# Kernel tuning notes

Measured on AMD Instinct MI355X. Metric: run time of the kernel, lower is better.

The kernel has to match this reference:

```python
import jax, jax.numpy as jnp
import numpy as np

CONF_THR = 0.3   # cfg.THRESHOLD_PREDICT_CONF
NMS_THR = 0.5    # cfg.THRESHOLD_PREDICT_NMS
TOPK = 500       # hard-coded topk(500) in forward


def _build_grid():
    # YOLOv3 @416: scales 13/26/52, 3 anchors each -> 10647 rows
    sizes = [13, 26, 52]
    anc = np.array([[10, 13], [16, 30], [33, 23], [30, 61], [62, 45], [59, 119],
                    [116, 90], [156, 198], [373, 326]], np.float32) / 416.0
    groups = [anc[6:9], anc[3:6], anc[0:3]]  # large anchors on coarse grid
    grids, anchors, fs = [], [], []
    for s, g in zip(sizes, groups):
        ys, xs = np.meshgrid(np.arange(s), np.arange(s), indexing='ij')
        gxy = np.stack([xs, ys], -1).astype(np.float32)          # [s,s,2]
        gxy = np.repeat(gxy.reshape(-1, 1, 2), 3, axis=1).reshape(-1, 2)
        grids.append(gxy)
        anchors.append(np.tile(g[None], (s * s, 1, 1)).reshape(-1, 2))
        fs.append(np.full((s * s * 3, 1), float(s), np.float32))
    return (np.concatenate(grids).astype(np.float32),
            np.concatenate(anchors).astype(np.float32),
            np.concatenate(fs).astype(np.float32))


def setup_inputs() -> dict:
    key = jax.random.key(0)
    k1, k2, k3 = jax.random.split(key, 3)
    B, A, C = 64, 10647, 80
    g, aw, fs = _build_grid()
    return {
        "pconf": jax.random.normal(k1, (B, A, 1), jnp.float32),
        "pcls": jax.random.normal(k2, (B, A, C), jnp.float32),
        "ptxywh": jax.random.normal(k3, (B, A, 4), jnp.float32),
        "grid_xy": jnp.asarray(g),
        "anchor_wh": jnp.asarray(aw),
        "fsize": jnp.asarray(fs),
    }


def _decode(ptxywh, grid_xy, anchor_wh, fsize):
    # boxes_decode4yolo3: sigmoid xy offset + cell, exp wh * anchor (all normalized)
    xy = (jax.nn.sigmoid(ptxywh[..., :2]) + grid_xy) / fsize   # [B,A,2]
    wh = jnp.exp(ptxywh[..., 2:]) * anchor_wh                  # [B,A,2]
    return jnp.concatenate([xy - 0.5 * wh, xy + 0.5 * wh], -1)  # ltrb


def _pairwise_iou(b):  # b: [K,4] ltrb
    area = jnp.maximum(b[:, 2] - b[:, 0], 0.) * jnp.maximum(b[:, 3] - b[:, 1], 0.)
    lt = jnp.maximum(b[:, None, :2], b[None, :, :2])
    rb = jnp.minimum(b[:, None, 2:], b[None, :, 2:])
    wh = jnp.maximum(rb - lt, 0.)
    inter = wh[..., 0] * wh[..., 1]
    return inter / (area[:, None] + area[None, :] - inter + 1e-9)


def _label_nms(boxes, labels, valid, thr):
    # boxes are pre-sorted by descending score (lax.top_k output order)
    K = boxes.shape[0]
    sup = (_pairwise_iou(boxes) > thr) & (labels[:, None] == labels[None, :])
    idx = jnp.arange(K)

    def body(suppressed, i):
        keep_i = valid[i] & ~suppressed[i]
        suppressed = suppressed | (keep_i & sup[i] & (idx > i))
        return suppressed, keep_i

    _, keep = jax.lax.scan(body, jnp.zeros(K, bool), idx)
    return keep


def reference(pconf, pcls, ptxywh, grid_xy, anchor_wh, fsize):
    B, A, _ = ptxywh.shape
    conf = jax.nn.sigmoid(pconf)[..., 0]            # [B,A]
    pc = jax.nn.sigmoid(pcls)                       # [B,A,C]
    cls_conf = pc.max(-1)
    plabels = pc.argmax(-1)
    pscores = cls_conf * conf                       # [B,A]

    vals, idx = jax.lax.top_k(pscores, TOPK)        # sorted desc, [B,K]
    valid = vals > CONF_THR                         # mask_pos AND mask_topk

    pltrb = _decode(ptxywh, grid_xy, anchor_wh, fsize)          # [B,A,4]
    boxes = jnp.take_along_axis(pltrb, idx[..., None], axis=1)  # [B,K,4]
    boxes = jnp.clip(boxes, 0.0, 1.0)
    labels = jnp.take_along_axis(plabels, idx, axis=1) + 1      # 1-based

    keep = jax.vmap(_label_nms, in_axes=(0, 0, 0, None))(boxes, labels, valid, NMS_THR)
    ids_batch = jnp.broadcast_to(jnp.arange(B)[:, None], (B, TOPK))
    return ids_batch, boxes, labels, vals, keep
```

## Files before the change

kernel.cpp:

```cpp
#include <hip/hip_runtime.h>
#include <math.h>

#define A_N 10647
#define C_N 80
#define K_N 500
#define CONF_THRF 0.3f
#define NMS_THRF 0.5f

#define NBUCK 1024
#define CAND_N 2048
#define CAND_TARGET 600

typedef float f32x4 __attribute__((ext_vector_type(4)));

__device__ __forceinline__ float sigmoid_ref(float x) {
    float e = expf(-x);
    return 1.0f / (1.0f + e);
}

__device__ __forceinline__ unsigned bucket_of(float v) {
    unsigned u = __float_as_uint(v) >> 20;
    return u > 1023u ? 1023u : u;
}

__device__ __forceinline__ unsigned long long shfl_u64(unsigned long long v, int src) {
    unsigned int lo = (unsigned int)v, hi = (unsigned int)(v >> 32);
    lo = __shfl(lo, src, 64);
    hi = __shfl(hi, src, 64);
    return ((unsigned long long)hi << 32) | (unsigned long long)lo;
}

__device__ __forceinline__ unsigned long long shfl_xor_u64(unsigned long long v, int mask) {
    unsigned int lo = (unsigned int)v, hi = (unsigned int)(v >> 32);
    lo = __shfl_xor(lo, mask, 64);
    hi = __shfl_xor(hi, mask, 64);
    return ((unsigned long long)hi << 32) | (unsigned long long)lo;
}

__device__ __forceinline__ void reduce_core(
    const f32x4 v[5], int sub, float& sbest, int& ibest) {
    float m = -3.4e38f;
    #pragma unroll
    for (int j = 0; j < 5; ++j)
        m = fmaxf(m, fmaxf(fmaxf(v[j][0], v[j][1]), fmaxf(v[j][2], v[j][3])));
    m = fmaxf(m, __shfl_xor(m, 1, 64));
    m = fmaxf(m, __shfl_xor(m, 2, 64));

    const float win = m - 1e-4f;
    int imin = 0x7FFFFFFF, cnt = 0;
    #pragma unroll
    for (int j = 0; j < 5; ++j) {
        #pragma unroll
        for (int t = 0; t < 4; ++t) {
            int idx = (sub + 4 * j) * 4 + t;
            if (v[j][t] == m && idx < imin) imin = idx;
            cnt += (v[j][t] >= win) ? 1 : 0;
        }
    }
    {
        int o = __shfl_xor(imin, 1, 64); imin = imin < o ? imin : o;
        o = __shfl_xor(imin, 2, 64);     imin = imin < o ? imin : o;
        cnt += __shfl_xor(cnt, 1, 64);
        cnt += __shfl_xor(cnt, 2, 64);
    }

    if (cnt >= 2) {
        unsigned long long key = 0ull;
        #pragma unroll
        for (int j = 0; j < 5; ++j) {
            #pragma unroll
            for (int t = 0; t < 4; ++t) {
                float x = v[j][t];
                if (x >= win) {
                    int idx = (sub + 4 * j) * 4 + t;
                    float s = sigmoid_ref(x);
                    unsigned long long k =
                        ((unsigned long long)__float_as_uint(s) << 32) |
                        (unsigned long long)(0xFFFFu - (unsigned)idx);
                    if (k > key) key = k;
                }
            }
        }
        unsigned long long o = shfl_xor_u64(key, 1); if (o > key) key = o;
        o = shfl_xor_u64(key, 2);                    if (o > key) key = o;
        sbest = __uint_as_float((unsigned int)(key >> 32));
        ibest = 0xFFFF - (int)(key & 0xFFFFull);
    } else {
        sbest = sigmoid_ref(m);
        ibest = imin;
    }
}

__global__ __launch_bounds__(1024) void ustar_kernel(
    const float* __restrict__ pconf,
    unsigned* __restrict__ ustar,
    unsigned* __restrict__ shist) {
    __shared__ unsigned hist[NBUCK];
    const int b = blockIdx.x, tid = threadIdx.x;
    hist[tid] = 0u;
    shist[(size_t)b * NBUCK + tid] = 0u;
    __syncthreads();
    for (int i = tid; i < A_N; i += 1024) {
        float ubv = sigmoid_ref(pconf[(size_t)b * A_N + i]);
        atomicAdd(&hist[bucket_of(ubv)], 1u);
    }
    __syncthreads();
    for (int d = 1; d < NBUCK; d <<= 1) {
        unsigned v = (tid + d < NBUCK) ? hist[tid + d] : 0u;
        __syncthreads();
        hist[tid] += v;
        __syncthreads();
    }
    if (hist[tid] >= CAND_TARGET && (tid == NBUCK - 1 || hist[tid + 1] < CAND_TARGET))
        ustar[b] = (unsigned)tid;
}

__global__ __launch_bounds__(256) void cand_kernel(
    const float* __restrict__ pconf,
    const float* __restrict__ pcls,
    float* __restrict__ scores,
    int* __restrict__ labels,
    const unsigned* __restrict__ ustar,
    unsigned* __restrict__ shist,
    int total) {
    const int sub = threadIdx.x & 3;
    const int g0 = (blockIdx.x * 256 + threadIdx.x) >> 2;
    const int gstride = (2048 * 256) >> 2;
    for (int r = g0; r < total; r += gstride) {
        unsigned b = (unsigned)r / A_N;
        float ub = sigmoid_ref(pconf[r]);
        if (bucket_of(ub) >= ustar[b]) {
            const f32x4* rp = (const f32x4*)(pcls + (size_t)r * C_N);
            f32x4 v[5];
            #pragma unroll
            for (int j = 0; j < 5; ++j) v[j] = rp[sub + 4 * j];
            float s; int ib;
            reduce_core(v, sub, s, ib);
            float sc = __fmul_rn(s, ub);
            if (sub == 0) {
                scores[r] = sc;
                labels[r] = ib;
                atomicAdd(&shist[(size_t)b * NBUCK + bucket_of(sc)], 1u);
            }
        }
    }
}

__global__ __launch_bounds__(1024) void tval_kernel(
    const unsigned* __restrict__ shist,
    float* __restrict__ tval) {
    __shared__ unsigned hist[NBUCK];
    const int b = blockIdx.x, tid = threadIdx.x;
    hist[tid] = shist[(size_t)b * NBUCK + tid];
    __syncthreads();
    for (int d = 1; d < NBUCK; d <<= 1) {
        unsigned v = (tid + d < NBUCK) ? hist[tid + d] : 0u;
        __syncthreads();
        hist[tid] += v;
        __syncthreads();
    }
    if (hist[tid] >= K_N && (tid == NBUCK - 1 || hist[tid + 1] < K_N))
        tval[b] = __uint_as_float(((unsigned)tid) << 20);
}

__global__ __launch_bounds__(256) void rest_kernel(
    const float* __restrict__ pconf,
    const float* __restrict__ pcls,
    float* __restrict__ scores,
    int* __restrict__ labels,
    const unsigned* __restrict__ ustar,
    const float* __restrict__ tval,
    int total) {
    const int sub = threadIdx.x & 3;
    const int g0 = (blockIdx.x * 256 + threadIdx.x) >> 2;
    const int gstride = (2048 * 256) >> 2;
    for (int r = g0; r < total; r += gstride) {
        unsigned b = (unsigned)r / A_N;
        float ub = sigmoid_ref(pconf[r]);
        unsigned u = bucket_of(ub);
        if (u >= ustar[b]) continue;
        if (ub >= tval[b]) {
            const f32x4* rp = (const f32x4*)(pcls + (size_t)r * C_N);
            f32x4 v[5];
            #pragma unroll
            for (int j = 0; j < 5; ++j) v[j] = rp[sub + 4 * j];
            float s; int ib;
            reduce_core(v, sub, s, ib);
            if (sub == 0) {
                scores[r] = __fmul_rn(s, ub);
                labels[r] = ib;
            }
        } else if (sub == 0) {
            scores[r] = 0.0f;
        }
    }
}

__global__ __launch_bounds__(1024) void topk_nms_kernel(
    const float* __restrict__ scores,
    const int* __restrict__ labels,
    const float* __restrict__ ptxywh,
    const float* __restrict__ grid_xy,
    const float* __restrict__ anchor_wh,
    const float* __restrict__ fsize,
    float* __restrict__ out, int B) {
    extern __shared__ unsigned char smem[];
    unsigned int* hist = (unsigned int*)smem;
    unsigned long long* cand = (unsigned long long*)(smem + 4096);
    unsigned int* cntp = (unsigned int*)(smem + 20480);
    unsigned int* Tp   = (unsigned int*)(smem + 20484);
    const int b = blockIdx.x;
    const int tid = threadIdx.x;
    const float* sb = scores + (size_t)b * A_N;

    hist[tid] = 0u;
    cand[tid] = 0ull;
    cand[tid + 1024] = 0ull;
    if (tid == 0) *cntp = 0u;
    __syncthreads();

    for (int i = tid; i < A_N; i += 1024) {
        unsigned int u = __float_as_uint(sb[i]) >> 20;
        atomicAdd(&hist[u], 1u);
    }
    __syncthreads();

    for (int d = 1; d < NBUCK; d <<= 1) {
        unsigned int v = (tid + d < NBUCK) ? hist[tid + d] : 0u;
        __syncthreads();
        hist[tid] += v;
        __syncthreads();
    }
    if (hist[tid] >= K_N && (tid == NBUCK - 1 || hist[tid + 1] < K_N)) *Tp = (unsigned)tid;
    __syncthreads();
    const unsigned int T = *Tp;
    __syncthreads();

    for (int i = tid; i < A_N; i += 1024) {
        unsigned int u = __float_as_uint(sb[i]);
        if ((u >> 20) >= T) {
            unsigned int slot = atomicAdd(cntp, 1u);
            if (slot < CAND_N)
                cand[slot] = ((unsigned long long)u << 32) |
                             (unsigned long long)(0xFFFFu - (unsigned)i);
        }
    }
    __syncthreads();

    for (int sz = 2; sz <= CAND_N; sz <<= 1) {
        for (int j = sz >> 1; j > 0; j >>= 1) {
            int i = ((tid & ~(j - 1)) << 1) | (tid & (j - 1));
            int l = i | j;
            unsigned long long a = cand[i];
            unsigned long long c = cand[l];
            bool descBlk = ((i & sz) == 0);
            if (descBlk ? (a < c) : (a > c)) { cand[i] = c; cand[l] = a; }
            __syncthreads();
        }
    }

    unsigned long long myk = 0ull;
    if (tid < K_N) myk = cand[tid];
    __syncthreads();

    float* bxL   = (float*)smem;
    float* areaL = (float*)(smem + 8000);
    int*   labL  = (int*)  (smem + 10000);
    float* valsL = (float*)(smem + 12000);
    unsigned long long* nzL   = (unsigned long long*)(smem + 14016);
    unsigned long long* keepL = (unsigned long long*)(smem + 14080);
    unsigned long long* supL  = (unsigned long long*)(smem + 14336);

    if (tid >= 512 && tid < 520) nzL[tid - 512] = 0ull;

    const size_t BK = (size_t)B * K_N;
    if (tid < K_N) {
        float scv = __uint_as_float((unsigned int)(myk >> 32));
        int idx = 0xFFFF - (int)(myk & 0xFFFFull);
        int lb = labels[(size_t)b * A_N + idx] + 1;
        const float* t4 = ptxywh + ((size_t)b * A_N + idx) * 4;
        float tx = t4[0], ty = t4[1], tw = t4[2], th = t4[3];
        float gx = grid_xy[idx * 2 + 0], gy = grid_xy[idx * 2 + 1];
        float aw = anchor_wh[idx * 2 + 0], ah = anchor_wh[idx * 2 + 1];
        float fs = fsize[idx];
        float cx = __fdiv_rn(__fadd_rn(sigmoid_ref(tx), gx), fs);
        float cy = __fdiv_rn(__fadd_rn(sigmoid_ref(ty), gy), fs);
        float wx = __fmul_rn(expf(tw), aw);
        float wy = __fmul_rn(expf(th), ah);
        float hx = __fmul_rn(0.5f, wx);
        float hy = __fmul_rn(0.5f, wy);
        float x0 = __fsub_rn(cx, hx), y0 = __fsub_rn(cy, hy);
        float x1 = __fadd_rn(cx, hx), y1 = __fadd_rn(cy, hy);
        x0 = fminf(fmaxf(x0, 0.0f), 1.0f);
        y0 = fminf(fmaxf(y0, 0.0f), 1.0f);
        x1 = fminf(fmaxf(x1, 0.0f), 1.0f);
        y1 = fminf(fmaxf(y1, 0.0f), 1.0f);
        float area = __fmul_rn(fmaxf(__fsub_rn(x1, x0), 0.0f),
                               fmaxf(__fsub_rn(y1, y0), 0.0f));
        bxL[tid * 4 + 0] = x0; bxL[tid * 4 + 1] = y0;
        bxL[tid * 4 + 2] = x1; bxL[tid * 4 + 3] = y1;
        areaL[tid] = area; labL[tid] = lb; valsL[tid] = scv;

        out[(size_t)b * K_N + tid] = (float)b;
        float* ob = out + BK + ((size_t)b * K_N + tid) * 4;
        ob[0] = x0; ob[1] = y0; ob[2] = x1; ob[3] = y1;
        out[5 * BK + (size_t)b * K_N + tid] = (float)lb;
        out[6 * BK + (size_t)b * K_N + tid] = scv;
    }
    __syncthreads();

    for (int task = tid; task < K_N * 8; task += 1024) {
        int i = task >> 3;
        int w = task & 7;
        float li = bxL[i * 4 + 0], ti = bxL[i * 4 + 1];
        float ri = bxL[i * 4 + 2], bi = bxL[i * 4 + 3];
        float ai = areaL[i];
        int lbi = labL[i];
        unsigned long long bits = 0ull;
        int j0 = w * 64;
        int jend = j0 + 64; if (jend > K_N) jend = K_N;
        int jst = j0 > i + 1 ? j0 : i + 1;
        for (int j = jst; j < jend; ++j) {
            if (labL[j] == lbi) {
                float lj = bxL[j * 4 + 0], tj = bxL[j * 4 + 1];
                float rj = bxL[j * 4 + 2], bj = bxL[j * 4 + 3];
                float ltx = fmaxf(li, lj), lty = fmaxf(ti, tj);
                float rbx = fminf(ri, rj), rby = fminf(bi, bj);
                float iw = fmaxf(__fsub_rn(rbx, ltx), 0.0f);
                float ih = fmaxf(__fsub_rn(rby, lty), 0.0f);
                float inter = __fmul_rn(iw, ih);
                float den = __fadd_rn(__fsub_rn(__fadd_rn(ai, areaL[j]), inter), 1e-9f);
                float iou = __fdiv_rn(inter, den);
                if (iou > NMS_THRF) bits |= (1ull << (j - j0));
            }
        }
        supL[i * 8 + w] = bits;
        if (bits) atomicOr(&nzL[i >> 6], 1ull << (i & 63));
    }
    __syncthreads();

    if (tid < 64) {
        const int lane = tid;
        unsigned long long supp = 0ull, keepm = 0ull;
        unsigned long long nzreg = (lane < 8) ? nzL[lane] : 0ull;
        #pragma unroll
        for (int t = 0; t < 8; ++t) {
            const int i0 = t * 64;
            int myi = i0 + lane;
            bool v = (myi < K_N) ? (valsL[myi] > CONF_THRF) : false;
            unsigned long long vword = __ballot(v);
            unsigned long long nzword = shfl_u64(nzreg, t);
            const int imax = (K_N - i0 < 64) ? (K_N - i0) : 64;
            for (int i2 = 0; i2 < imax; ++i2) {
                unsigned long long sw = shfl_u64(supp, t);
                bool keep_i = ((vword >> i2) & 1ull) && !((sw >> i2) & 1ull);
                if (keep_i) {
                    if (lane == t) keepm |= (1ull << i2);
                    if ((nzword >> i2) & 1ull) {
                        if (lane < 8) supp |= supL[(i0 + i2) * 8 + lane];
                    }
                }
            }
        }
        if (lane < 8) keepL[lane] = keepm;
    }
    __syncthreads();

    if (tid < K_N) {
        unsigned long long kw = keepL[tid >> 6];
        out[7 * BK + (size_t)b * K_N + tid] = (float)((kw >> (tid & 63)) & 1ull);
    }
}

extern "C" void kernel_launch(void* const* d_in, const int* in_sizes, int n_in,
                              void* d_out, int out_size, void* d_ws, size_t ws_size,
                              hipStream_t stream) {
    const float* pconf     = (const float*)d_in[0];
    const float* pcls      = (const float*)d_in[1];
    const float* ptxywh    = (const float*)d_in[2];
    const float* grid_xy   = (const float*)d_in[3];
    const float* anchor_wh = (const float*)d_in[4];
    const float* fsize     = (const float*)d_in[5];
    int total = in_sizes[0];
    int B = total / A_N;
    if (B <= 0) return;

    float*    scores = (float*)d_ws;
    int*      labls  = (int*)((char*)d_ws + (size_t)total * 4);
    unsigned* shist  = (unsigned*)((char*)d_ws + (size_t)total * 8);
    unsigned* ustar  = shist + (size_t)B * NBUCK;
    float*    tval   = (float*)(ustar + B);
    float*    out    = (float*)d_out;

    hipLaunchKernelGGL(ustar_kernel, dim3(B), dim3(1024), 0, stream,
                       pconf, ustar, shist);
    hipLaunchKernelGGL(cand_kernel, dim3(2048), dim3(256), 0, stream,
                       pconf, pcls, scores, labls, ustar, shist, total);
    hipLaunchKernelGGL(tval_kernel, dim3(B), dim3(1024), 0, stream,
                       shist, tval);
    hipLaunchKernelGGL(rest_kernel, dim3(2048), dim3(256), 0, stream,
                       pconf, pcls, scores, labls, ustar, tval, total);
    hipLaunchKernelGGL(topk_nms_kernel, dim3(B), dim3(1024), 46592, stream,
                       scores, labls, ptxywh, grid_xy, anchor_wh, fsize, out, B);
}
```

Baseline: 177.9 us.

## Compact candidate row indices into per-batch lists before class scoring

The per-batch histogram kernels now also build compacted index lists of rows that pass the bucket threshold, and the scoring kernels iterate over those lists instead of scanning all rows and branching. This removes the divergent full scans where most lanes idle, so the class-row loads only go to work-dense wavefronts. In exchange, the per-batch 1024-thread kernels do a second pass over pconf, the scoring kernels still launch enough threads to cover every row and most exit early, and list order depends on atomics.

```diff
diff --git a/kernel.cpp b/kernel.cpp
--- a/kernel.cpp
+++ b/kernel.cpp
@@ -91,18 +91,22 @@
     }
 }
 
-__global__ __launch_bounds__(1024) void ustar_kernel(
+__global__ __launch_bounds__(1024) void ustar_compact_kernel(
     const float* __restrict__ pconf,
+    unsigned* __restrict__ shist,
     unsigned* __restrict__ ustar,
-    unsigned* __restrict__ shist) {
+    int* __restrict__ list1,
+    unsigned* __restrict__ count1) {
     __shared__ unsigned hist[NBUCK];
+    __shared__ unsigned lcnt, ustarL;
     const int b = blockIdx.x, tid = threadIdx.x;
     hist[tid] = 0u;
     shist[(size_t)b * NBUCK + tid] = 0u;
+    if (tid == 0) lcnt = 0u;
     __syncthreads();
     for (int i = tid; i < A_N; i += 1024) {
-        float ubv = sigmoid_ref(pconf[(size_t)b * A_N + i]);
-        atomicAdd(&hist[bucket_of(ubv)], 1u);
+        float ub = sigmoid_ref(pconf[(size_t)b * A_N + i]);
+        atomicAdd(&hist[bucket_of(ub)], 1u);
     }
     __syncthreads();
     for (int d = 1; d < NBUCK; d <<= 1) {
@@ -112,46 +116,70 @@
         __syncthreads();
     }
     if (hist[tid] >= CAND_TARGET && (tid == NBUCK - 1 || hist[tid + 1] < CAND_TARGET))
-        ustar[b] = (unsigned)tid;
-}
-
-__global__ __launch_bounds__(256) void cand_kernel(
+        ustarL = (unsigned)tid;
+    __syncthreads();
+    const unsigned u = ustarL;
+    if (tid == 0) ustar[b] = u;
+    for (int i = tid; i < A_N; i += 1024) {
+        int r = b * A_N + i;
+        float ub = sigmoid_ref(pconf[r]);
+        if (bucket_of(ub) >= u) {
+            unsigned slot = atomicAdd(&lcnt, 1u);
+            list1[(size_t)b * A_N + slot] = r;
+        }
+    }
+    __syncthreads();
+    if (tid == 0) count1[b] = lcnt;
+}
+
+template<bool DO_HIST>
+__global__ __launch_bounds__(256) void score_list_kernel(
     const float* __restrict__ pconf,
     const float* __restrict__ pcls,
     float* __restrict__ scores,
     int* __restrict__ labels,
-    const unsigned* __restrict__ ustar,
+    const int* __restrict__ list,
+    const unsigned* __restrict__ count,
     unsigned* __restrict__ shist,
     int total) {
     const int sub = threadIdx.x & 3;
     const int g0 = (blockIdx.x * 256 + threadIdx.x) >> 2;
     const int gstride = (2048 * 256) >> 2;
-    for (int r = g0; r < total; r += gstride) {
-        unsigned b = (unsigned)r / A_N;
+    for (int idx = g0; idx < total; idx += gstride) {
+        int b = idx / A_N;
+        int k = idx - b * A_N;
+        if (k >= (int)count[b]) continue;
+        int r = list[idx];
         float ub = sigmoid_ref(pconf[r]);
-        if (bucket_of(ub) >= ustar[b]) {
-            const f32x4* rp = (const f32x4*)(pcls + (size_t)r * C_N);
-            f32x4 v[5];
-            #pragma unroll
-            for (int j = 0; j < 5; ++j) v[j] = rp[sub + 4 * j];
-            float s; int ib;
-            reduce_core(v, sub, s, ib);
-            float sc = __fmul_rn(s, ub);
-            if (sub == 0) {
-                scores[r] = sc;
-                labels[r] = ib;
+        const f32x4* rp = (const f32x4*)(pcls + (size_t)r * C_N);
+        f32x4 v[5];
+        #pragma unroll
+        for (int j = 0; j < 5; ++j) v[j] = rp[sub + 4 * j];
+        float s; int ib;
+        reduce_core(v, sub, s, ib);
+        float sc = __fmul_rn(s, ub);
+        if (sub == 0) {
+            scores[r] = sc;
+            labels[r] = ib;
+            if (DO_HIST)
                 atomicAdd(&shist[(size_t)b * NBUCK + bucket_of(sc)], 1u);
-            }
-        }
-    }
-}
-
-__global__ __launch_bounds__(1024) void tval_kernel(
+        }
+    }
+}
+
+__global__ __launch_bounds__(1024) void tval_compact_kernel(
+    const float* __restrict__ pconf,
     const unsigned* __restrict__ shist,
-    float* __restrict__ tval) {
+    const unsigned* __restrict__ ustar,
+    float* __restrict__ scores,
+    int* __restrict__ list2,
+    unsigned* __restrict__ count2) {
     __shared__ unsigned hist[NBUCK];
+    __shared__ unsigned lcnt;
+    __shared__ float tL;
     const int b = blockIdx.x, tid = threadIdx.x;
     hist[tid] = shist[(size_t)b * NBUCK + tid];
+    if (tid == 0) lcnt = 0u;
     __syncthreads();
     for (int d = 1; d < NBUCK; d <<= 1) {
         unsigned v = (tid + d < NBUCK) ? hist[tid + d] : 0u;
@@ -160,40 +188,24 @@
         __syncthreads();
     }
     if (hist[tid] >= K_N && (tid == NBUCK - 1 || hist[tid + 1] < K_N))
-        tval[b] = __uint_as_float(((unsigned)tid) << 20);
-}
-
-__global__ __launch_bounds__(256) void rest_kernel(
-    const float* __restrict__ pconf,
-    const float* __restrict__ pcls,
-    float* __restrict__ scores,
-    int* __restrict__ labels,
-    const unsigned* __restrict__ ustar,
-    const float* __restrict__ tval,
-    int total) {
-    const int sub = threadIdx.x & 3;
-    const int g0 = (blockIdx.x * 256 + threadIdx.x) >> 2;
-    const int gstride = (2048 * 256) >> 2;
-    for (int r = g0; r < total; r += gstride) {
-        unsigned b = (unsigned)r / A_N;
+        tL = __uint_as_float(((unsigned)tid) << 20);
+    __syncthreads();
+    const float t = tL;
+    const unsigned u = ustar[b];
+    for (int i = tid; i < A_N; i += 1024) {
+        int r = b * A_N + i;
         float ub = sigmoid_ref(pconf[r]);
-        unsigned u = bucket_of(ub);
-        if (u >= ustar[b]) continue;
-        if (ub >= tval[b]) {
-            const f32x4* rp = (const f32x4*)(pcls + (size_t)r * C_N);
-            f32x4 v[5];
-            #pragma unroll
-            for (int j = 0; j < 5; ++j) v[j] = rp[sub + 4 * j];
-            float s; int ib;
-            reduce_core(v, sub, s, ib);
-            if (sub == 0) {
-                scores[r] = __fmul_rn(s, ub);
-                labels[r] = ib;
-            }
-        } else if (sub == 0) {
+        unsigned bk = bucket_of(ub);
+        if (bk >= u) continue;
+        if (ub >= t) {
+            unsigned slot = atomicAdd(&lcnt, 1u);
+            list2[(size_t)b * A_N + slot] = r;
+        } else {
             scores[r] = 0.0f;
         }
     }
+    __syncthreads();
+    if (tid == 0) count2[b] = lcnt;
 }
 
 __global__ __launch_bounds__(1024) void topk_nms_kernel(
@@ -385,21 +397,25 @@
     int B = total / A_N;
     if (B <= 0) return;
 
-    float*    scores = (float*)d_ws;
-    int*      labls  = (int*)((char*)d_ws + (size_t)total * 4);
-    unsigned* shist  = (unsigned*)((char*)d_ws + (size_t)total * 8);
-    unsigned* ustar  = shist + (size_t)B * NBUCK;
-    float*    tval   = (float*)(ustar + B);
+    char* w = (char*)d_ws;
+    float*    scores = (float*)w;                      w += (size_t)total * 4;
+    int*      labls  = (int*)w;                        w += (size_t)total * 4;
+    int*      list1  = (int*)w;                        w += (size_t)total * 4;
+    int*      list2  = (int*)w;                        w += (size_t)total * 4;
+    unsigned* shist  = (unsigned*)w;                   w += (size_t)B * NBUCK * 4;
+    unsigned* ustar  = (unsigned*)w;                   w += (size_t)B * 4;
+    unsigned* count1 = (unsigned*)w;                   w += (size_t)B * 4;
+    unsigned* count2 = (unsigned*)w;
     float*    out    = (float*)d_out;
 
-    hipLaunchKernelGGL(ustar_kernel, dim3(B), dim3(1024), 0, stream,
-                       pconf, ustar, shist);
-    hipLaunchKernelGGL(cand_kernel, dim3(2048), dim3(256), 0, stream,
-                       pconf, pcls, scores, labls, ustar, shist, total);
-    hipLaunchKernelGGL(tval_kernel, dim3(B), dim3(1024), 0, stream,
-                       shist, tval);
-    hipLaunchKernelGGL(rest_kernel, dim3(2048), dim3(256), 0, stream,
-                       pconf, pcls, scores, labls, ustar, tval, total);
+    hipLaunchKernelGGL(ustar_compact_kernel, dim3(B), dim3(1024), 0, stream,
+                       pconf, shist, ustar, list1, count1);
+    hipLaunchKernelGGL((score_list_kernel<true>), dim3(2048), dim3(256), 0, stream,
+                       pconf, pcls, scores, labls, list1, count1, shist, total);
+    hipLaunchKernelGGL(tval_compact_kernel, dim3(B), dim3(1024), 0, stream,
+                       pconf, shist, ustar, scores, list2, count2);
+    hipLaunchKernelGGL((score_list_kernel<false>), dim3(2048), dim3(256), 0, stream,
+                       pconf, pcls, scores, labls, list2, count2, (unsigned*)nullptr, total);
     hipLaunchKernelGGL(topk_nms_kernel, dim3(B), dim3(1024), 46592, stream,
                        scores, labls, ptxywh, grid_xy, anchor_wh, fsize, out, B);
 }
```

Result: faster. 159.7 us (-10.3%).
